# Kernel tuning notes

Hardware: AMD Instinct MI355X
Metric: run time of the kernel (lower is better)

## Reference

```python
import jax, jax.numpy as jnp
import numpy as np

HIDDEN = 2048
INTER = 768
N_EXPERTS = 16
TOP_K = 2
B, S = 4, 2048


def setup_inputs() -> dict:
    key = jax.random.key(0)
    ks = jax.random.split(key, 5)
    scale = 0.02
    return {
        "hidden_states": jax.random.normal(ks[0], (B, S, HIDDEN), dtype=jnp.float32),
        # nn.Linear weight layout: [out_features, in_features]
        "gate_w": jax.random.normal(ks[1], (N_EXPERTS, HIDDEN), dtype=jnp.float32) * scale,
        "w_gate": jax.random.normal(ks[2], (N_EXPERTS, INTER, HIDDEN), dtype=jnp.float32) * scale,
        "w_up": jax.random.normal(ks[3], (N_EXPERTS, INTER, HIDDEN), dtype=jnp.float32) * scale,
        "w_down": jax.random.normal(ks[4], (N_EXPERTS, HIDDEN, INTER), dtype=jnp.float32) * scale,
    }


def _moe_forward(hidden_states, gate_w, w_gate, w_up, w_down):
    b, s, h = hidden_states.shape
    x = hidden_states.reshape(-1, h)                      # [T, H]
    t = x.shape[0]
    logits = x @ gate_w.T                                 # [T, E]
    probs = jax.nn.softmax(logits, axis=-1)
    top_vals, top_idx = jax.lax.top_k(probs, TOP_K)       # [T, K]
    top_vals = top_vals / jnp.sum(top_vals, axis=-1, keepdims=True)
    # combine weights per token per expert (zero if not routed)
    comb = jnp.zeros((t, N_EXPERTS), dtype=x.dtype)
    comb = comb.at[jnp.arange(t)[:, None], top_idx].add(top_vals)  # [T, E]

    out = jnp.zeros_like(x)
    for e in range(N_EXPERTS):  # small fixed loop over experts
        g = x @ w_gate[e].T                               # [T, I]
        u = x @ w_up[e].T                                 # [T, I]
        y = (jax.nn.silu(g) * u) @ w_down[e].T            # [T, H]
        out = out + comb[:, e:e + 1] * y
    return out.reshape(b, s, h)


def reference(hidden_states, gate_w, w_gate, w_up, w_down):
    return _moe_forward(hidden_states, gate_w, w_gate, w_up, w_down)
```

## Files before the change

kernel.cpp:

```cpp
#include <hip/hip_runtime.h>
#include <hip/hip_bf16.h>

#define NTOK 8192
#define HID 2048
#define INTER 768
#define NEXP 16

typedef __bf16 bf16x8 __attribute__((ext_vector_type(8)));
typedef float f32x4 __attribute__((ext_vector_type(4)));

typedef const __attribute__((address_space(1))) void gvoid_t;
typedef __attribute__((address_space(3))) void lvoid_t;

static __device__ __forceinline__ void load_lds16(const void* g, void* l) {
  __builtin_amdgcn_global_load_lds((gvoid_t*)g, (lvoid_t*)l, 16, 0, 0);
}

static __device__ __forceinline__ unsigned short f2bf(float f) {
  unsigned int u = __float_as_uint(f);
  u += 0x7FFFu + ((u >> 16) & 1u);
  return (unsigned short)(u >> 16);
}

static __device__ __forceinline__ float bf2f(unsigned short b) {
  return __uint_as_float(((unsigned int)b) << 16);
}

__global__ __launch_bounds__(256) void cvt_kernel(const float* __restrict__ src,
                                                  unsigned short* __restrict__ dst, int n) {
  int i = (blockIdx.x * 256 + threadIdx.x) * 4;
  int stride = gridDim.x * 256 * 4;
  for (; i < n; i += stride) {
    float4 v = *reinterpret_cast<const float4*>(src + i);
    ushort4 o;
    o.x = f2bf(v.x); o.y = f2bf(v.y); o.z = f2bf(v.z); o.w = f2bf(v.w);
    *reinterpret_cast<ushort4*>(dst + i) = o;
  }
}

__global__ __launch_bounds__(256) void router_kernel(const float* __restrict__ x,
                                                     const float* __restrict__ gw,
                                                     int* __restrict__ te,
                                                     float* __restrict__ tw,
                                                     unsigned short* __restrict__ Xb) {
  const int lane = threadIdx.x & 63;
  const int wid = threadIdx.x >> 6;
  const int t0 = (blockIdx.x * 4 + wid) * 2;
  const float4* xa = reinterpret_cast<const float4*>(x + (size_t)t0 * HID);
  const float4* xb = xa + HID / 4;
  const float4* g4 = reinterpret_cast<const float4*>(gw);

  float4 va[8], vb[8];
#pragma unroll
  for (int j = 0; j < 8; ++j) {
    va[j] = xa[lane + 64 * j];
    vb[j] = xb[lane + 64 * j];
  }
  ushort4* oa = reinterpret_cast<ushort4*>(Xb + (size_t)t0 * HID);
  ushort4* ob = oa + HID / 4;
#pragma unroll
  for (int j = 0; j < 8; ++j) {
    ushort4 u;
    u.x = f2bf(va[j].x); u.y = f2bf(va[j].y); u.z = f2bf(va[j].z); u.w = f2bf(va[j].w);
    oa[lane + 64 * j] = u;
    u.x = f2bf(vb[j].x); u.y = f2bf(vb[j].y); u.z = f2bf(vb[j].z); u.w = f2bf(vb[j].w);
    ob[lane + 64 * j] = u;
  }

  float accA[NEXP], accB[NEXP];
#pragma unroll
  for (int e = 0; e < NEXP; ++e) { accA[e] = 0.f; accB[e] = 0.f; }
#pragma unroll
  for (int e = 0; e < NEXP; ++e) {
#pragma unroll
    for (int j = 0; j < 8; ++j) {
      float4 g = g4[e * (HID / 4) + lane + 64 * j];
      accA[e] += va[j].x * g.x + va[j].y * g.y + va[j].z * g.z + va[j].w * g.w;
      accB[e] += vb[j].x * g.x + vb[j].y * g.y + vb[j].z * g.z + vb[j].w * g.w;
    }
  }
#pragma unroll
  for (int e = 0; e < NEXP; ++e) {
#pragma unroll
    for (int m = 32; m >= 1; m >>= 1) {
      accA[e] += __shfl_xor(accA[e], m);
      accB[e] += __shfl_xor(accB[e], m);
    }
  }
  if (lane == 0) {
#pragma unroll
    for (int k = 0; k < 2; ++k) {
      const float* acc = k ? accB : accA;
      int t = t0 + k;
      float b0 = -1e30f; int i0 = 0;
#pragma unroll
      for (int e = 0; e < NEXP; ++e) { if (acc[e] > b0) { b0 = acc[e]; i0 = e; } }
      float b1 = -1e30f; int i1 = 0;
#pragma unroll
      for (int e = 0; e < NEXP; ++e) { if (e != i0 && acc[e] > b1) { b1 = acc[e]; i1 = e; } }
      float w0 = 1.f / (1.f + __expf(b1 - b0));
      te[2 * t] = i0; te[2 * t + 1] = i1;
      tw[2 * t] = w0; tw[2 * t + 1] = 1.f - w0;
    }
  }
}

__global__ __launch_bounds__(256) void build_kernel(
    const int* __restrict__ te, const float* __restrict__ tw,
    int* __restrict__ counts, int* __restrict__ offsets,
    int* __restrict__ tok_flat, float* __restrict__ w_flat,
    int* __restrict__ tok_slot,
    int* __restrict__ tile_map, int* __restrict__ n_tiles) {
  __shared__ int lds_cnt[NEXP][257];
  __shared__ int lds_off[NEXP];
  const int tid = threadIdx.x;
  const int lane = tid & 63;
  const int wv = tid >> 6;

  int cnt[NEXP];
#pragma unroll
  for (int ex = 0; ex < NEXP; ++ex) cnt[ex] = 0;
  for (int i = 0; i < 64; ++i) {
    int e = te[tid * 64 + i];
#pragma unroll
    for (int ex = 0; ex < NEXP; ++ex) cnt[ex] += (e == ex) ? 1 : 0;
  }
#pragma unroll
  for (int ex = 0; ex < NEXP; ++ex) lds_cnt[ex][tid] = cnt[ex];
  __syncthreads();

  for (int ex = wv * 4; ex < wv * 4 + 4; ++ex) {
    int carry = 0;
    for (int c = 0; c < 4; ++c) {
      int v = lds_cnt[ex][c * 64 + lane];
      int s = v;
#pragma unroll
      for (int d = 1; d < 64; d <<= 1) {
        int o = __shfl_up(s, d);
        if (lane >= d) s += o;
      }
      lds_cnt[ex][c * 64 + lane] = carry + s - v;
      carry += __shfl(s, 63);
    }
    if (lane == 0) lds_cnt[ex][256] = carry;
  }
  __syncthreads();

  if (tid == 0) {
    int run = 0, nt = 0;
    for (int e = 0; e < NEXP; ++e) {
      int tot = lds_cnt[e][256];
      counts[e] = tot;
      offsets[e] = run;
      lds_off[e] = run;
      for (int m0 = 0; m0 < tot; m0 += 128) tile_map[nt++] = (e << 16) | m0;
      run += tot;
    }
    *n_tiles = nt;
  }
  __syncthreads();

  int base[NEXP];
#pragma unroll
  for (int ex = 0; ex < NEXP; ++ex) base[ex] = lds_off[ex] + lds_cnt[ex][tid];
  for (int i = 0; i < 64; ++i) {
    int idx = tid * 64 + i;
    int e = te[idx];
    float w = tw[idx];
    int pos = 0;
#pragma unroll
    for (int ex = 0; ex < NEXP; ++ex) {
      if (e == ex) { pos = base[ex]; base[ex] = pos + 1; }
    }
    tok_flat[pos] = idx >> 1;
    w_flat[pos] = w;
    tok_slot[idx] = pos;
  }
}

__global__ __launch_bounds__(256, 2) void gemm_gu_kernel(
    const unsigned short* __restrict__ Xb,
    const unsigned short* __restrict__ Wg,
    const unsigned short* __restrict__ Wu,
    const int* __restrict__ counts, const int* __restrict__ offsets,
    const int* __restrict__ tok_flat,
    const int* __restrict__ tile_map, const int* __restrict__ n_tiles,
    unsigned short* __restrict__ Hf) {
  const int bid = blockIdx.x;
  const int cpx = gridDim.x >> 3;
  const int wg = (bid & 7) * cpx + (bid >> 3);
  const int y = wg / 6;
  if (y >= *n_tiles) return;
  const int xb = wg - y * 6;
  const int tm = tile_map[y];
  const int e = tm >> 16, m0 = tm & 0xFFFF;
  const int cnt = counts[e];
  const int off = offsets[e];
  const int n0 = xb * 128;

  __shared__ __align__(16) unsigned short As0[128 * 32], As1[128 * 32];
  __shared__ __align__(16) unsigned short Bg0[128 * 32], Bg1[128 * 32];
  __shared__ __align__(16) unsigned short Bu0[128 * 32], Bu1[128 * 32];

  const int tid = threadIdx.x;
  const int lane = tid & 63;
  const int wid = tid >> 6;
  const int rl = tid >> 2;
  const int srcc = ((tid & 3) ^ ((tid >> 3) & 3)) * 8;
  const int d0 = tid * 8;
  const int d1 = d0 + 64 * 32;

  const int r0 = m0 + rl, r1 = r0 + 64;
  const int s0 = (r0 < cnt) ? off + r0 : off;
  const int s1 = (r1 < cnt) ? off + r1 : off;
  const unsigned short* aptr0 = Xb + (size_t)tok_flat[s0] * HID + srcc;
  const unsigned short* aptr1 = Xb + (size_t)tok_flat[s1] * HID + srcc;
  const unsigned short* gptr0 = Wg + ((size_t)e * INTER + n0 + rl) * HID + srcc;
  const unsigned short* gptr1 = gptr0 + (size_t)64 * HID;
  const unsigned short* uptr0 = Wu + ((size_t)e * INTER + n0 + rl) * HID + srcc;
  const unsigned short* uptr1 = uptr0 + (size_t)64 * HID;

  f32x4 zero = {0.f, 0.f, 0.f, 0.f};
  f32x4 accG[4][4], accU[4][4];
#pragma unroll
  for (int i = 0; i < 4; ++i)
#pragma unroll
    for (int j = 0; j < 4; ++j) { accG[i][j] = zero; accU[i][j] = zero; }

  const int wm = (wid >> 1) * 64;
  const int wn = (wid & 1) * 64;
  const int fr = lane & 15;
  const int cs = (((lane >> 4) ^ ((lane >> 1) & 3)) * 8);

#define STAGE_GU(AS, BGS, BUS, kt)           \
  {                                          \
    load_lds16(aptr0 + (kt), (AS) + d0);     \
    load_lds16(aptr1 + (kt), (AS) + d1);     \
    load_lds16(gptr0 + (kt), (BGS) + d0);    \
    load_lds16(gptr1 + (kt), (BGS) + d1);    \
    load_lds16(uptr0 + (kt), (BUS) + d0);    \
    load_lds16(uptr1 + (kt), (BUS) + d1);    \
  }

#define COMPUTE_GU(AS, BGS, BUS)                                                       \
  {                                                                                    \
    bf16x8 af[4], bg[4], bu[4];                                                        \
    _Pragma("unroll") for (int i = 0; i < 4; ++i) {                                    \
      af[i] = *reinterpret_cast<const bf16x8*>((AS) + (wm + i * 16 + fr) * 32 + cs);   \
      bg[i] = *reinterpret_cast<const bf16x8*>((BGS) + (wn + i * 16 + fr) * 32 + cs);  \
      bu[i] = *reinterpret_cast<const bf16x8*>((BUS) + (wn + i * 16 + fr) * 32 + cs);  \
    }                                                                                  \
    _Pragma("unroll") for (int i = 0; i < 4; ++i)                                      \
      _Pragma("unroll") for (int j = 0; j < 4; ++j) {                                  \
        accG[i][j] = __builtin_amdgcn_mfma_f32_16x16x32_bf16(af[i], bg[j], accG[i][j], 0, 0, 0); \
        accU[i][j] = __builtin_amdgcn_mfma_f32_16x16x32_bf16(af[i], bu[j], accU[i][j], 0, 0, 0); \
      }                                                                                \
  }

#pragma unroll 1
  for (int kt = 0; kt < HID; kt += 64) {
    STAGE_GU(As0, Bg0, Bu0, kt);
    STAGE_GU(As1, Bg1, Bu1, kt + 32);
    __syncthreads();
    COMPUTE_GU(As0, Bg0, Bu0);
    COMPUTE_GU(As1, Bg1, Bu1);
    __syncthreads();
  }
#undef STAGE_GU
#undef COMPUTE_GU

  const int lr = (lane >> 4) * 4;
  const int lc = lane & 15;
#pragma unroll
  for (int i = 0; i < 4; ++i) {
#pragma unroll
    for (int r = 0; r < 4; ++r) {
      int m = wm + i * 16 + lr + r;
      if (m0 + m < cnt) {
        size_t base = (size_t)(off + m0 + m) * INTER + (size_t)(n0 + wn + lc);
#pragma unroll
        for (int j = 0; j < 4; ++j) {
          float g = accG[i][j][r];
          float u = accU[i][j][r];
          float h = g / (1.f + __expf(-g)) * u;
          Hf[base + j * 16] = f2bf(h);
        }
      }
    }
  }
}

__global__ __launch_bounds__(256, 3) void gemm_y_kernel(
    const unsigned short* __restrict__ Hf,
    const unsigned short* __restrict__ Wd,
    const int* __restrict__ counts, const int* __restrict__ offsets,
    const float* __restrict__ w_flat,
    const int* __restrict__ tile_map, const int* __restrict__ n_tiles,
    unsigned short* __restrict__ Yf) {
  const int bid = blockIdx.x;
  const int cpx = gridDim.x >> 3;
  const int wg = (bid & 7) * cpx + (bid >> 3);
  const int y = wg / 16;
  if (y >= *n_tiles) return;
  const int xb = wg - y * 16;
  const int tm = tile_map[y];
  const int e = tm >> 16, m0 = tm & 0xFFFF;
  const int cnt = counts[e];
  const int off = offsets[e];
  const int n0 = xb * 128;

  __shared__ __align__(16) unsigned short As0[128 * 32], As1[128 * 32];
  __shared__ __align__(16) unsigned short Bs0[128 * 32], Bs1[128 * 32];

  const int tid = threadIdx.x;
  const int lane = tid & 63;
  const int wid = tid >> 6;
  const int rl = tid >> 2;
  const int srcc = ((tid & 3) ^ ((tid >> 3) & 3)) * 8;
  const int d0 = tid * 8;
  const int d1 = d0 + 64 * 32;

  const int r0 = m0 + rl, r1 = r0 + 64;
  const int s0 = (r0 < cnt) ? off + r0 : off;
  const int s1 = (r1 < cnt) ? off + r1 : off;
  const unsigned short* aptr0 = Hf + (size_t)s0 * INTER + srcc;
  const unsigned short* aptr1 = Hf + (size_t)s1 * INTER + srcc;
  const unsigned short* bptr0 = Wd + ((size_t)e * HID + n0 + rl) * INTER + srcc;
  const unsigned short* bptr1 = bptr0 + (size_t)64 * INTER;

  f32x4 zero = {0.f, 0.f, 0.f, 0.f};
  f32x4 acc[4][4];
#pragma unroll
  for (int i = 0; i < 4; ++i)
#pragma unroll
    for (int j = 0; j < 4; ++j) acc[i][j] = zero;

  const int wm = (wid >> 1) * 64;
  const int wn = (wid & 1) * 64;
  const int fr = lane & 15;
  const int cs = (((lane >> 4) ^ ((lane >> 1) & 3)) * 8);

#define STAGE_Y(AS, BS, kt)               \
  {                                       \
    load_lds16(aptr0 + (kt), (AS) + d0);  \
    load_lds16(aptr1 + (kt), (AS) + d1);  \
    load_lds16(bptr0 + (kt), (BS) + d0);  \
    load_lds16(bptr1 + (kt), (BS) + d1);  \
  }

#define COMPUTE_Y(AS, BS)                                                              \
  {                                                                                    \
    bf16x8 af[4], bf_[4];                                                              \
    _Pragma("unroll") for (int i = 0; i < 4; ++i) {                                    \
      af[i] = *reinterpret_cast<const bf16x8*>((AS) + (wm + i * 16 + fr) * 32 + cs);   \
      bf_[i] = *reinterpret_cast<const bf16x8*>((BS) + (wn + i * 16 + fr) * 32 + cs);  \
    }                                                                                  \
    _Pragma("unroll") for (int i = 0; i < 4; ++i)                                      \
      _Pragma("unroll") for (int j = 0; j < 4; ++j)                                    \
        acc[i][j] = __builtin_amdgcn_mfma_f32_16x16x32_bf16(af[i], bf_[j], acc[i][j], 0, 0, 0); \
  }

#pragma unroll 1
  for (int kt = 0; kt < INTER; kt += 64) {
    STAGE_Y(As0, Bs0, kt);
    STAGE_Y(As1, Bs1, kt + 32);
    __syncthreads();
    COMPUTE_Y(As0, Bs0);
    COMPUTE_Y(As1, Bs1);
    __syncthreads();
  }
#undef STAGE_Y
#undef COMPUTE_Y

  const int lr = (lane >> 4) * 4;
  const int lc = lane & 15;
#pragma unroll
  for (int i = 0; i < 4; ++i) {
#pragma unroll
    for (int r = 0; r < 4; ++r) {
      int m = wm + i * 16 + lr + r;
      if (m0 + m < cnt) {
        int slot = off + m0 + m;
        float w = w_flat[slot];
        size_t base = (size_t)slot * HID + (size_t)(n0 + wn + lc);
#pragma unroll
        for (int j = 0; j < 4; ++j) Yf[base + j * 16] = f2bf(w * acc[i][j][r]);
      }
    }
  }
}

__global__ __launch_bounds__(256) void combine_kernel(const unsigned short* __restrict__ Yf,
                                                      const int* __restrict__ tok_slot,
                                                      float* __restrict__ out) {
  const int t = blockIdx.x;
  const int c = threadIdx.x * 8;
  const int s0 = tok_slot[2 * t];
  const int s1 = tok_slot[2 * t + 1];
  const ushort4* p0 = reinterpret_cast<const ushort4*>(Yf + (size_t)s0 * HID + c);
  const ushort4* p1 = reinterpret_cast<const ushort4*>(Yf + (size_t)s1 * HID + c);
  ushort4 a0 = p0[0], a1 = p0[1];
  ushort4 b0 = p1[0], b1 = p1[1];
  float4 o0, o1;
  o0.x = bf2f(a0.x) + bf2f(b0.x);
  o0.y = bf2f(a0.y) + bf2f(b0.y);
  o0.z = bf2f(a0.z) + bf2f(b0.z);
  o0.w = bf2f(a0.w) + bf2f(b0.w);
  o1.x = bf2f(a1.x) + bf2f(b1.x);
  o1.y = bf2f(a1.y) + bf2f(b1.y);
  o1.z = bf2f(a1.z) + bf2f(b1.z);
  o1.w = bf2f(a1.w) + bf2f(b1.w);
  float4* op = reinterpret_cast<float4*>(out + (size_t)t * HID + c);
  op[0] = o0;
  op[1] = o1;
}

extern "C" void kernel_launch(void* const* d_in, const int* in_sizes, int n_in,
                              void* d_out, int out_size, void* d_ws, size_t ws_size,
                              hipStream_t stream) {
  const float* x  = (const float*)d_in[0];
  const float* gw = (const float*)d_in[1];
  const float* wg = (const float*)d_in[2];
  const float* wu = (const float*)d_in[3];
  const float* wd = (const float*)d_in[4];
  float* out = (float*)d_out;
  char* ws = (char*)d_ws;

  int*   counts   = (int*)(ws + 0);
  int*   offsets  = (int*)(ws + 128);
  int*   n_tiles  = (int*)(ws + 192);
  int*   tile_map = (int*)(ws + 256);
  int*   te       = (int*)(ws + 1024);
  float* tw       = (float*)(ws + 66560);
  int*   tok_flat = (int*)(ws + 132096);
  float* w_flat   = (float*)(ws + 197632);
  unsigned short* Xb  = (unsigned short*)(ws + 263168);
  unsigned short* Wgb = (unsigned short*)(ws + 33817600);
  unsigned short* Wub = (unsigned short*)(ws + 84149248);
  unsigned short* Wdb = (unsigned short*)(ws + 134480896);
  unsigned short* Hf  = (unsigned short*)(ws + 184812544);
  int*   tok_slot = (int*)(ws + 209978368);
  unsigned short* Yf  = Wgb;

  cvt_kernel<<<2048, 256, 0, stream>>>(wg, Wgb, NEXP * INTER * HID);
  cvt_kernel<<<2048, 256, 0, stream>>>(wu, Wub, NEXP * INTER * HID);
  cvt_kernel<<<2048, 256, 0, stream>>>(wd, Wdb, NEXP * HID * INTER);

  router_kernel<<<NTOK / 8, 256, 0, stream>>>(x, gw, te, tw, Xb);
  build_kernel<<<1, 256, 0, stream>>>(te, tw, counts, offsets, tok_flat, w_flat,
                                      tok_slot, tile_map, n_tiles);

  gemm_gu_kernel<<<144 * 6, 256, 0, stream>>>(
      Xb, Wgb, Wub, counts, offsets, tok_flat, tile_map, n_tiles, Hf);
  gemm_y_kernel<<<144 * 16, 256, 0, stream>>>(
      Hf, Wdb, counts, offsets, w_flat, tile_map, n_tiles, Yf);
  combine_kernel<<<NTOK, 256, 0, stream>>>(Yf, tok_slot, out);
}
```

Before: 449.8 us.

## Software-pipeline GEMM K-loops with overlapped LDS staging and merge weight-convert launches

Both grouped GEMM kernels now prefetch the next half-tile into one LDS buffer while computing on the other. Each __syncthreads is replaced by an explicit vmcnt(0) wait plus s_barrier, so global-to-LDS loads overlap MFMA work instead of running serially before it. The three fp32-to-bf16 weight conversion launches are merged into one 3D-grid launch with fewer blocks per tensor. The pipeline leans on the waitcnt/barrier ordering being correct for the buffer reuse, and the merged launch cuts per-tensor parallelism.

```diff
diff --git a/kernel.cpp b/kernel.cpp
--- a/kernel.cpp
+++ b/kernel.cpp
@@ -26,8 +26,16 @@
   return __uint_as_float(((unsigned int)b) << 16);
 }
 
-__global__ __launch_bounds__(256) void cvt_kernel(const float* __restrict__ src,
-                                                  unsigned short* __restrict__ dst, int n) {
+#define SYNC_PIPE                                     \
+  asm volatile("s_waitcnt vmcnt(0)" ::: "memory");    \
+  __builtin_amdgcn_s_barrier();
+
+__global__ __launch_bounds__(256) void cvt3_kernel(
+    const float* __restrict__ s0, const float* __restrict__ s1, const float* __restrict__ s2,
+    unsigned short* __restrict__ dst0, unsigned short* __restrict__ dst1,
+    unsigned short* __restrict__ dst2, int n) {
+  const float* src = (blockIdx.y == 0) ? s0 : (blockIdx.y == 1) ? s1 : s2;
+  unsigned short* dst = (blockIdx.y == 0) ? dst0 : (blockIdx.y == 1) ? dst1 : dst2;
   int i = (blockIdx.x * 256 + threadIdx.x) * 4;
   int stride = gridDim.x * 256 * 4;
   for (; i < n; i += stride) {
@@ -257,14 +265,16 @@
       }                                                                                \
   }
 
+  STAGE_GU(As0, Bg0, Bu0, 0);
+  SYNC_PIPE
 #pragma unroll 1
   for (int kt = 0; kt < HID; kt += 64) {
-    STAGE_GU(As0, Bg0, Bu0, kt);
     STAGE_GU(As1, Bg1, Bu1, kt + 32);
-    __syncthreads();
     COMPUTE_GU(As0, Bg0, Bu0);
+    SYNC_PIPE
+    if (kt + 64 < HID) STAGE_GU(As0, Bg0, Bu0, kt + 64);
     COMPUTE_GU(As1, Bg1, Bu1);
-    __syncthreads();
+    SYNC_PIPE
   }
 #undef STAGE_GU
 #undef COMPUTE_GU
@@ -360,14 +370,16 @@
         acc[i][j] = __builtin_amdgcn_mfma_f32_16x16x32_bf16(af[i], bf_[j], acc[i][j], 0, 0, 0); \
   }
 
+  STAGE_Y(As0, Bs0, 0);
+  SYNC_PIPE
 #pragma unroll 1
   for (int kt = 0; kt < INTER; kt += 64) {
-    STAGE_Y(As0, Bs0, kt);
     STAGE_Y(As1, Bs1, kt + 32);
-    __syncthreads();
     COMPUTE_Y(As0, Bs0);
+    SYNC_PIPE
+    if (kt + 64 < INTER) STAGE_Y(As0, Bs0, kt + 64);
     COMPUTE_Y(As1, Bs1);
-    __syncthreads();
+    SYNC_PIPE
   }
 #undef STAGE_Y
 #undef COMPUTE_Y
@@ -442,9 +454,8 @@
   int*   tok_slot = (int*)(ws + 209978368);
   unsigned short* Yf  = Wgb;
 
-  cvt_kernel<<<2048, 256, 0, stream>>>(wg, Wgb, NEXP * INTER * HID);
-  cvt_kernel<<<2048, 256, 0, stream>>>(wu, Wub, NEXP * INTER * HID);
-  cvt_kernel<<<2048, 256, 0, stream>>>(wd, Wdb, NEXP * HID * INTER);
+  cvt3_kernel<<<dim3(1024, 3), 256, 0, stream>>>(wg, wu, wd, Wgb, Wub, Wdb,
+                                                 NEXP * INTER * HID);
 
   router_kernel<<<NTOK / 8, 256, 0, stream>>>(x, gw, te, tw, Xb);
   build_kernel<<<1, 256, 0, stream>>>(te, tw, counts, offsets, tok_flat, w_flat,
```

Result: no change. 453.9 us (+0.9%).

## Widen down-projection tile to 128x256 and merge weight conversion launches

Applied to the files above, without the earlier changes.

The down-projection GEMM now computes a 128x256 output tile per block, with two 128-column B sub-tiles sharing one staged A tile. This halves the A reloads and the block count, at the cost of doubling accumulator registers and cutting occupancy to 2 blocks per SIMD. The three fp32-to-bf16 weight conversion launches are also merged into a single launch with a 3-row grid, which removes launch overhead.

```diff
diff --git a/kernel.cpp b/kernel.cpp
--- a/kernel.cpp
+++ b/kernel.cpp
@@ -26,8 +26,12 @@
   return __uint_as_float(((unsigned int)b) << 16);
 }
 
-__global__ __launch_bounds__(256) void cvt_kernel(const float* __restrict__ src,
-                                                  unsigned short* __restrict__ dst, int n) {
+__global__ __launch_bounds__(256) void cvt3_kernel(
+    const float* __restrict__ s0, const float* __restrict__ s1, const float* __restrict__ s2,
+    unsigned short* __restrict__ dst0, unsigned short* __restrict__ dst1,
+    unsigned short* __restrict__ dst2, int n) {
+  const float* src = (blockIdx.y == 0) ? s0 : (blockIdx.y == 1) ? s1 : s2;
+  unsigned short* dst = (blockIdx.y == 0) ? dst0 : (blockIdx.y == 1) ? dst1 : dst2;
   int i = (blockIdx.x * 256 + threadIdx.x) * 4;
   int stride = gridDim.x * 256 * 4;
   for (; i < n; i += stride) {
@@ -290,7 +294,7 @@
   }
 }
 
-__global__ __launch_bounds__(256, 3) void gemm_y_kernel(
+__global__ __launch_bounds__(256, 2) void gemm_y2_kernel(
     const unsigned short* __restrict__ Hf,
     const unsigned short* __restrict__ Wd,
     const int* __restrict__ counts, const int* __restrict__ offsets,
@@ -300,17 +304,18 @@
   const int bid = blockIdx.x;
   const int cpx = gridDim.x >> 3;
   const int wg = (bid & 7) * cpx + (bid >> 3);
-  const int y = wg / 16;
+  const int y = wg / 8;
   if (y >= *n_tiles) return;
-  const int xb = wg - y * 16;
+  const int xb = wg - y * 8;
   const int tm = tile_map[y];
   const int e = tm >> 16, m0 = tm & 0xFFFF;
   const int cnt = counts[e];
   const int off = offsets[e];
-  const int n0 = xb * 128;
+  const int n0 = xb * 256;
 
   __shared__ __align__(16) unsigned short As0[128 * 32], As1[128 * 32];
-  __shared__ __align__(16) unsigned short Bs0[128 * 32], Bs1[128 * 32];
+  __shared__ __align__(16) unsigned short Bp0[128 * 32], Bp1[128 * 32];
+  __shared__ __align__(16) unsigned short Bq0[128 * 32], Bq1[128 * 32];
 
   const int tid = threadIdx.x;
   const int lane = tid & 63;
@@ -325,52 +330,59 @@
   const int s1 = (r1 < cnt) ? off + r1 : off;
   const unsigned short* aptr0 = Hf + (size_t)s0 * INTER + srcc;
   const unsigned short* aptr1 = Hf + (size_t)s1 * INTER + srcc;
-  const unsigned short* bptr0 = Wd + ((size_t)e * HID + n0 + rl) * INTER + srcc;
-  const unsigned short* bptr1 = bptr0 + (size_t)64 * INTER;
+  const unsigned short* pptr0 = Wd + ((size_t)e * HID + n0 + rl) * INTER + srcc;
+  const unsigned short* pptr1 = pptr0 + (size_t)64 * INTER;
+  const unsigned short* qptr0 = Wd + ((size_t)e * HID + n0 + 128 + rl) * INTER + srcc;
+  const unsigned short* qptr1 = qptr0 + (size_t)64 * INTER;
 
   f32x4 zero = {0.f, 0.f, 0.f, 0.f};
-  f32x4 acc[4][4];
+  f32x4 accP[4][4], accQ[4][4];
 #pragma unroll
   for (int i = 0; i < 4; ++i)
 #pragma unroll
-    for (int j = 0; j < 4; ++j) acc[i][j] = zero;
+    for (int j = 0; j < 4; ++j) { accP[i][j] = zero; accQ[i][j] = zero; }
 
   const int wm = (wid >> 1) * 64;
   const int wn = (wid & 1) * 64;
   const int fr = lane & 15;
   const int cs = (((lane >> 4) ^ ((lane >> 1) & 3)) * 8);
 
-#define STAGE_Y(AS, BS, kt)               \
-  {                                       \
-    load_lds16(aptr0 + (kt), (AS) + d0);  \
-    load_lds16(aptr1 + (kt), (AS) + d1);  \
-    load_lds16(bptr0 + (kt), (BS) + d0);  \
-    load_lds16(bptr1 + (kt), (BS) + d1);  \
-  }
-
-#define COMPUTE_Y(AS, BS)                                                              \
+#define STAGE_Y2(AS, BPS, BQS, kt)           \
+  {                                          \
+    load_lds16(aptr0 + (kt), (AS) + d0);     \
+    load_lds16(aptr1 + (kt), (AS) + d1);     \
+    load_lds16(pptr0 + (kt), (BPS) + d0);    \
+    load_lds16(pptr1 + (kt), (BPS) + d1);    \
+    load_lds16(qptr0 + (kt), (BQS) + d0);    \
+    load_lds16(qptr1 + (kt), (BQS) + d1);    \
+  }
+
+#define COMPUTE_Y2(AS, BPS, BQS)                                                       \
   {                                                                                    \
-    bf16x8 af[4], bf_[4];                                                              \
+    bf16x8 af[4], bp[4], bq[4];                                                        \
     _Pragma("unroll") for (int i = 0; i < 4; ++i) {                                    \
       af[i] = *reinterpret_cast<const bf16x8*>((AS) + (wm + i * 16 + fr) * 32 + cs);   \
-      bf_[i] = *reinterpret_cast<const bf16x8*>((BS) + (wn + i * 16 + fr) * 32 + cs);  \
+      bp[i] = *reinterpret_cast<const bf16x8*>((BPS) + (wn + i * 16 + fr) * 32 + cs);  \
+      bq[i] = *reinterpret_cast<const bf16x8*>((BQS) + (wn + i * 16 + fr) * 32 + cs);  \
     }                                                                                  \
     _Pragma("unroll") for (int i = 0; i < 4; ++i)                                      \
-      _Pragma("unroll") for (int j = 0; j < 4; ++j)                                    \
-        acc[i][j] = __builtin_amdgcn_mfma_f32_16x16x32_bf16(af[i], bf_[j], acc[i][j], 0, 0, 0); \
+      _Pragma("unroll") for (int j = 0; j < 4; ++j) {                                  \
+        accP[i][j] = __builtin_amdgcn_mfma_f32_16x16x32_bf16(af[i], bp[j], accP[i][j], 0, 0, 0); \
+        accQ[i][j] = __builtin_amdgcn_mfma_f32_16x16x32_bf16(af[i], bq[j], accQ[i][j], 0, 0, 0); \
+      }                                                                                \
   }
 
 #pragma unroll 1
   for (int kt = 0; kt < INTER; kt += 64) {
-    STAGE_Y(As0, Bs0, kt);
-    STAGE_Y(As1, Bs1, kt + 32);
+    STAGE_Y2(As0, Bp0, Bq0, kt);
+    STAGE_Y2(As1, Bp1, Bq1, kt + 32);
     __syncthreads();
-    COMPUTE_Y(As0, Bs0);
-    COMPUTE_Y(As1, Bs1);
+    COMPUTE_Y2(As0, Bp0, Bq0);
+    COMPUTE_Y2(As1, Bp1, Bq1);
     __syncthreads();
   }
-#undef STAGE_Y
-#undef COMPUTE_Y
+#undef STAGE_Y2
+#undef COMPUTE_Y2
 
   const int lr = (lane >> 4) * 4;
   const int lc = lane & 15;
@@ -382,9 +394,12 @@
       if (m0 + m < cnt) {
         int slot = off + m0 + m;
         float w = w_flat[slot];
-        size_t base = (size_t)slot * HID + (size_t)(n0 + wn + lc);
-#pragma unroll
-        for (int j = 0; j < 4; ++j) Yf[base + j * 16] = f2bf(w * acc[i][j][r]);
+        size_t base0 = (size_t)slot * HID + (size_t)(n0 + wn + lc);
+#pragma unroll
+        for (int j = 0; j < 4; ++j) {
+          Yf[base0 + j * 16] = f2bf(w * accP[i][j][r]);
+          Yf[base0 + 128 + j * 16] = f2bf(w * accQ[i][j][r]);
+        }
       }
     }
   }
@@ -442,17 +457,15 @@
   int*   tok_slot = (int*)(ws + 209978368);
   unsigned short* Yf  = Wgb;
 
-  cvt_kernel<<<2048, 256, 0, stream>>>(wg, Wgb, NEXP * INTER * HID);
-  cvt_kernel<<<2048, 256, 0, stream>>>(wu, Wub, NEXP * INTER * HID);
-  cvt_kernel<<<2048, 256, 0, stream>>>(wd, Wdb, NEXP * HID * INTER);
-
+  cvt3_kernel<<<dim3(1024, 3), 256, 0, stream>>>(wg, wu, wd, Wgb, Wub, Wdb,
+                                                 NEXP * INTER * HID);
   router_kernel<<<NTOK / 8, 256, 0, stream>>>(x, gw, te, tw, Xb);
   build_kernel<<<1, 256, 0, stream>>>(te, tw, counts, offsets, tok_flat, w_flat,
                                       tok_slot, tile_map, n_tiles);
 
   gemm_gu_kernel<<<144 * 6, 256, 0, stream>>>(
       Xb, Wgb, Wub, counts, offsets, tok_flat, tile_map, n_tiles, Hf);
-  gemm_y_kernel<<<144 * 16, 256, 0, stream>>>(
+  gemm_y2_kernel<<<144 * 8, 256, 0, stream>>>(
       Hf, Wdb, counts, offsets, w_flat, tile_map, n_tiles, Yf);
   combine_kernel<<<NTOK, 256, 0, stream>>>(Yf, tok_slot, out);
 }
```

Measured after the change: 457.4 us. No clear change (+1.7%).
